# Performance work log

Hardware: AMD Instinct MI355X
Metric: run time of the kernel (lower is better)

Reference implementation:

```python
import jax, jax.numpy as jnp
import numpy as np

D_MODEL = 1024
N_HEADS = 16
HEAD_DIM = D_MODEL // N_HEADS


def setup_inputs() -> dict:
    key = jax.random.key(0)
    k1, k2, k3, k4, k5 = jax.random.split(key, 5)
    s = 1.0 / np.sqrt(D_MODEL)
    return {
        "x": jax.random.normal(k1, (2, 2048, D_MODEL), dtype=jnp.float32),
        "w_qkv": jax.random.normal(k2, (D_MODEL, 3 * D_MODEL), dtype=jnp.float32) * s,
        "b_qkv": jax.random.normal(k3, (3 * D_MODEL,), dtype=jnp.float32) * 0.02,
        "w_proj": jax.random.normal(k4, (D_MODEL, D_MODEL), dtype=jnp.float32) * s,
        "b_proj": jax.random.normal(k5, (D_MODEL,), dtype=jnp.float32) * 0.02,
    }


def reference(x, w_qkv, b_qkv, w_proj, b_proj):
    B, S, D = x.shape
    H, Hd = N_HEADS, HEAD_DIM
    qkv = x @ w_qkv + b_qkv                       # [B,S,3D]
    q, k, v = jnp.split(qkv, 3, axis=-1)
    # split heads -> [B,H,S,Hd]
    q = q.reshape(B, S, H, Hd).transpose(0, 2, 1, 3)
    k = k.reshape(B, S, H, Hd).transpose(0, 2, 1, 3)
    v = v.reshape(B, S, H, Hd).transpose(0, 2, 1, 3)
    scale = 1.0 / jnp.sqrt(jnp.asarray(Hd, dtype=x.dtype))
    scores = jnp.einsum("bhqd,bhkd->bhqk", q, k) * scale  # [B,H,S,S]
    causal = jnp.tril(jnp.ones((S, S), dtype=bool))
    scores = jnp.where(causal, scores, jnp.asarray(-jnp.inf, dtype=scores.dtype))
    attn = jax.nn.softmax(scores, axis=-1)
    out = jnp.einsum("bhqk,bhkd->bhqd", attn, v)  # [B,H,S,Hd]
    out = out.transpose(0, 2, 1, 3).reshape(B, S, D)
    return out @ w_proj + b_proj
```

## Files before the change

kernel.cpp:

```cpp
#include <hip/hip_runtime.h>


typedef float f32x4 __attribute__((ext_vector_type(4)));
typedef float f32x16 __attribute__((ext_vector_type(16)));
typedef short bf16x8 __attribute__((ext_vector_type(8)));

#if __has_builtin(__builtin_amdgcn_exp2f)
#define EXP2(x) __builtin_amdgcn_exp2f(x)
#else
#define EXP2(x) exp2f(x)
#endif

__device__ __forceinline__ unsigned short f2bf(float f) {
  union { float f; unsigned u; } v; v.f = f;
  unsigned u = v.u + 0x7fffu + ((v.u >> 16) & 1u);
  return (unsigned short)(u >> 16);
}

__device__ __forceinline__ void async_load16(const void* g, void* lds) {
  __builtin_amdgcn_global_load_lds(
      (const __attribute__((address_space(1))) void*)g,
      (__attribute__((address_space(3))) void*)lds, 16, 0, 0);
}

__global__ void f32_to_bf16_kernel(const float* __restrict__ in,
                                   unsigned short* __restrict__ out, int n) {
  int i = (blockIdx.x * 256 + threadIdx.x) * 4;
  if (i < n) {
    float4 f = *(const float4*)(in + i);
    ushort4 o;
    o.x = f2bf(f.x); o.y = f2bf(f.y); o.z = f2bf(f.z); o.w = f2bf(f.w);
    *(ushort4*)(out + i) = o;
  }
}

__global__ void transpose_f32_bf16_kernel(const float* __restrict__ in,
                                          unsigned short* __restrict__ out,
                                          int K, int N) {
  __shared__ float tile[32][33];
  int n0 = blockIdx.x * 32, k0 = blockIdx.y * 32;
  int tx = threadIdx.x, ty = threadIdx.y;
#pragma unroll
  for (int i = ty; i < 32; i += 8)
    tile[i][tx] = in[(size_t)(k0 + i) * N + (n0 + tx)];
  __syncthreads();
#pragma unroll
  for (int i = ty; i < 32; i += 8)
    out[(size_t)(n0 + i) * K + (k0 + tx)] = f2bf(tile[tx][i]);
}

template <int MI, int NI>
__device__ __forceinline__ void gemm_mainloop(
    const unsigned short* __restrict__ A,
    const unsigned short* __restrict__ BT,
    int K, int mBlk, int nBlk,
    unsigned short* As, unsigned short* Bs,
    f32x4 (&acc)[MI][NI], int lane, int wave)
{
  const int l16 = lane & 15, quad = lane >> 4;
  const int mW = (wave >> 1) * MI * 16;
  const int nW = (wave & 1) * NI * 16;
  constexpr int AROWS = 2 * MI * 16;
  constexpr int BROWS = 2 * NI * 16;
  constexpr int AINST = AROWS / 64;
  constexpr int BINST = BROWS / 64;
  const int rl = lane >> 2;
  const int cl = (lane & 3) * 8;

  for (int k0 = 0; k0 < K; k0 += 32) {
    __syncthreads();
#pragma unroll
    for (int t = 0; t < AINST; ++t) {
      const int rbase = wave * (AROWS / 4) + t * 16;
      async_load16(A + (size_t)(mBlk + rbase + rl) * K + k0 + cl, &As[rbase * 32]);
    }
#pragma unroll
    for (int t = 0; t < BINST; ++t) {
      const int rbase = wave * (BROWS / 4) + t * 16;
      async_load16(BT + (size_t)(nBlk + rbase + rl) * K + k0 + cl, &Bs[rbase * 32]);
    }
    __syncthreads();

    bf16x8 af[MI], bf[NI];
#pragma unroll
    for (int i = 0; i < MI; ++i)
      af[i] = *(const bf16x8*)&As[(mW + i * 16 + l16) * 32 + quad * 8];
#pragma unroll
    for (int j = 0; j < NI; ++j)
      bf[j] = *(const bf16x8*)&Bs[(nW + j * 16 + l16) * 32 + quad * 8];
#pragma unroll
    for (int i = 0; i < MI; ++i)
#pragma unroll
      for (int j = 0; j < NI; ++j)
        acc[i][j] = __builtin_amdgcn_mfma_f32_16x16x32_bf16(af[i], bf[j], acc[i][j], 0, 0, 0);
  }
}

__global__ __launch_bounds__(512, 2) void qkv_gemm_kernel(
    const unsigned short* __restrict__ A,
    const unsigned short* __restrict__ WT,
    const float* __restrict__ bias,
    unsigned short* __restrict__ QKV)
{
  __shared__ __align__(16) unsigned short Al[2][2][256][32];
  __shared__ __align__(16) unsigned short Bl[2][2][256][32];
  const int lane = threadIdx.x & 63;
  const int wave = threadIdx.x >> 6;
  const int l16 = lane & 15, quad = lane >> 4;
  const int wm = wave >> 2, wn = wave & 3;

  const int bid = blockIdx.x;
  const int xcd = bid & 7, rb = bid >> 3;
  const int bx = (xcd & 3) * 4 + (rb & 3);
  const int by = (xcd >> 2) * 6 + (rb >> 2);
  const int mBlk = bx * 256, nBlk = by * 256;

  const int srow = wave * 32 + (lane >> 2);
  const int scol = lane & 3;

  auto stage = [&](const unsigned short* __restrict__ G, int gRow0,
                   unsigned short (*L)[32], int kOff) {
#pragma unroll
    for (int i = 0; i < 2; ++i) {
      const int row = srow + i * 16;
      const int c = scol ^ ((row >> 1) & 3);
      async_load16(G + (size_t)(gRow0 + row) * 1024 + kOff + c * 8,
                   &L[wave * 32 + i * 16][0]);
    }
  };

  auto rdA = [&](int buf, int kh, int mi) -> bf16x8 {
    const int r = wm * 128 + mi * 16 + l16;
    return *(const bf16x8*)&Al[buf][kh][r][(quad ^ ((r >> 1) & 3)) * 8];
  };
  auto rdB = [&](int buf, int kh, int n) -> bf16x8 {
    const int r = wn * 64 + n * 16 + l16;
    return *(const bf16x8*)&Bl[buf][kh][r][(quad ^ ((r >> 1) & 3)) * 8];
  };

  f32x4 acc[8][4];
  const f32x4 z4 = {0.f, 0.f, 0.f, 0.f};
#pragma unroll
  for (int i = 0; i < 8; ++i)
#pragma unroll
    for (int j = 0; j < 4; ++j) acc[i][j] = z4;

  stage(A, mBlk, Al[0][0], 0);
  stage(WT, nBlk, Bl[0][0], 0);
  stage(A, mBlk, Al[0][1], 32);
  stage(WT, nBlk, Bl[0][1], 32);
  asm volatile("s_waitcnt vmcnt(4)\n\ts_barrier" ::: "memory");

  for (int t = 0; t < 16; ++t) {
    const int cur = t & 1, nxt = cur ^ 1;
    const int tn = (t + 1 < 16) ? t + 1 : 15;
    const int kO = tn * 64;
    bf16x8 bf[4], af[4];

    stage(A, mBlk, Al[nxt][0], kO);
#pragma unroll
    for (int n = 0; n < 4; ++n) bf[n] = rdB(cur, 0, n);
#pragma unroll
    for (int i = 0; i < 4; ++i) af[i] = rdA(cur, 0, i);
    asm volatile("s_barrier" ::: "memory");
    __builtin_amdgcn_s_setprio(1);
#pragma unroll
    for (int i = 0; i < 4; ++i)
#pragma unroll
      for (int n = 0; n < 4; ++n)
        acc[i][n] = __builtin_amdgcn_mfma_f32_16x16x32_bf16(af[i], bf[n], acc[i][n], 0, 0, 0);
    __builtin_amdgcn_s_setprio(0);
    asm volatile("s_barrier" ::: "memory");

    stage(WT, nBlk, Bl[nxt][0], kO);
#pragma unroll
    for (int i = 0; i < 4; ++i) af[i] = rdA(cur, 0, 4 + i);
    asm volatile("s_barrier" ::: "memory");
    __builtin_amdgcn_s_setprio(1);
#pragma unroll
    for (int i = 0; i < 4; ++i)
#pragma unroll
      for (int n = 0; n < 4; ++n)
        acc[4 + i][n] = __builtin_amdgcn_mfma_f32_16x16x32_bf16(af[i], bf[n], acc[4 + i][n], 0, 0, 0);
    __builtin_amdgcn_s_setprio(0);
    asm volatile("s_waitcnt vmcnt(4)\n\ts_barrier" ::: "memory");

    stage(A, mBlk, Al[nxt][1], kO + 32);
#pragma unroll
    for (int n = 0; n < 4; ++n) bf[n] = rdB(cur, 1, n);
#pragma unroll
    for (int i = 0; i < 4; ++i) af[i] = rdA(cur, 1, i);
    asm volatile("s_barrier" ::: "memory");
    __builtin_amdgcn_s_setprio(1);
#pragma unroll
    for (int i = 0; i < 4; ++i)
#pragma unroll
      for (int n = 0; n < 4; ++n)
        acc[i][n] = __builtin_amdgcn_mfma_f32_16x16x32_bf16(af[i], bf[n], acc[i][n], 0, 0, 0);
    __builtin_amdgcn_s_setprio(0);
    asm volatile("s_barrier" ::: "memory");

    stage(WT, nBlk, Bl[nxt][1], kO + 32);
#pragma unroll
    for (int i = 0; i < 4; ++i) af[i] = rdA(cur, 1, 4 + i);
    asm volatile("s_barrier" ::: "memory");
    __builtin_amdgcn_s_setprio(1);
#pragma unroll
    for (int i = 0; i < 4; ++i)
#pragma unroll
      for (int n = 0; n < 4; ++n)
        acc[4 + i][n] = __builtin_amdgcn_mfma_f32_16x16x32_bf16(af[i], bf[n], acc[4 + i][n], 0, 0, 0);
    __builtin_amdgcn_s_setprio(0);
    asm volatile("s_waitcnt vmcnt(4)\n\ts_barrier" ::: "memory");
  }
  asm volatile("s_waitcnt vmcnt(0)" ::: "memory");

  const int m0 = mBlk + wm * 128;
  const int n0 = nBlk + wn * 64;
  const int whichW = n0 >> 10;
  const int bb = m0 >> 11;
  const int sBase = (m0 & 2047);
  const size_t planeE = (size_t)2 * 16 * 2048 * 64;

  if (whichW == 2) {
    unsigned short* Vb = QKV + 2 * planeE;
#pragma unroll
    for (int j = 0; j < 4; ++j) {
      const int rem = (n0 & 1023) + j * 16 + l16;
      const int hh = rem >> 6, hd = rem & 63;
      const float bv = bias[n0 + j * 16 + l16];
      unsigned short* col = Vb + (((size_t)bb * 16 + hh) * 64 + hd) * 2048;
#pragma unroll
      for (int i = 0; i < 8; ++i) {
        unsigned short pk[4];
#pragma unroll
        for (int r = 0; r < 4; ++r) pk[r] = f2bf(acc[i][j][r] + bv);
        *(ushort4*)&col[sBase + i * 16 + quad * 4] = *(ushort4*)pk;
      }
    }
  } else {
    const float scale = (whichW == 0) ? 0.18033688011112042f : 1.0f;
#pragma unroll
    for (int j = 0; j < 4; ++j) {
      const int n = n0 + j * 16 + l16;
      const float bv = bias[n];
      const int rem = n & 1023;
      const int hh = rem >> 6, hd = rem & 63;
      unsigned short* pl = QKV + (size_t)whichW * planeE +
                           (((size_t)bb * 16 + hh) * 2048) * 64 + hd;
#pragma unroll
      for (int r = 0; r < 4; ++r) {
        const int s = sBase + (quad * 4 + r);
#pragma unroll
        for (int i = 0; i < 8; ++i)
          pl[(size_t)(s + i * 16) * 64] = f2bf((acc[i][j][r] + bv) * scale);
      }
    }
  }
}

__global__ __launch_bounds__(256, 2) void attn_kernel(
    const unsigned short* __restrict__ QKV,
    unsigned short* __restrict__ AO)
{
  __shared__ __align__(16) unsigned short Ks[3 * 64 * 64];
  __shared__ __align__(16) unsigned short Vs[3 * 64 * 64];
  const int lane = threadIdx.x & 63;
  const int wave = threadIdx.x >> 6;
  const int l31 = lane & 31;
  const int hi  = lane >> 5;

  const int lin  = blockIdx.x;
  const int xcd  = lin & 7;
  const int slot = lin >> 3;
  const int col  = xcd * 4 + (slot >> 4);
  const int b = col >> 4, h = col & 15;
  const int qg = (slot < 32) ? (slot & 15) : (15 - (slot & 15));
  const int qw = qg * 128 + wave * 32;

  const size_t planeE = (size_t)2 * 16 * 2048 * 64;
  const size_t bhS = ((size_t)b * 16 + h) * (size_t)(2048 * 64);
  const unsigned short* Q   = QKV + bhS;
  const unsigned short* Kg  = QKV + planeE + bhS;
  const unsigned short* VTg = QKV + 2 * planeE + bhS;

  bf16x8 qf_[4];
#pragma unroll
  for (int t = 0; t < 4; ++t)
    qf_[t] = *(const bf16x8*)(Q + (size_t)(qw + l31) * 64 + t * 16 + hi * 8);

  bf16x8 onesf;
#pragma unroll
  for (int i = 0; i < 8; ++i) onesf[i] = (short)0x3F80;

  f32x16 O[2], Osum;
#pragma unroll
  for (int r = 0; r < 16; ++r) { O[0][r] = 0.f; O[1][r] = 0.f; Osum[r] = 0.f; }

  const int tbase = (wave & 1) * 4;
  const bool doV = wave >= 2;

  auto stage = [&](int tileIdx, int bufIdx) {
    const int kt = tileIdx * 64;
    unsigned short* Kb = Ks + bufIdx * 4096;
    unsigned short* Vb = Vs + bufIdx * 4096;
#pragma unroll
    for (int i = 0; i < 4; ++i) {
      const int t = tbase + i;
      const int s = t * 64 + lane;
      const int row = s >> 3;
      const int c = (s & 7) ^ (row & 7);
      if (doV)
        async_load16(VTg + (size_t)row * 2048 + kt + c * 8, Vb + t * 512);
      else
        async_load16(Kg + (size_t)(kt + row) * 64 + c * 8, Kb + t * 512);
    }
  };

  const int nt = qg * 2 + 2;
  stage(0, 0);
  stage(1, 1);
  for (int ti = 0; ti < nt; ++ti) {
    asm volatile("s_waitcnt vmcnt(4)\n\ts_barrier" ::: "memory");
    const int tn = (ti + 2 < nt) ? ti + 2 : nt - 1;
    stage(tn, (ti + 2) % 3);
    const int kt = ti * 64;
    const unsigned short* Kb = Ks + (ti % 3) * 4096;
    const unsigned short* Vb = Vs + (ti % 3) * 4096;

    if (kt <= qw + 31) {
      const bool dmask = (kt + 63 > qw);
#pragma unroll
      for (int kg = 0; kg < 2; ++kg) {
        const int krow = kg * 32 + l31;
        const int ks7 = krow & 7;
        bf16x8 ka[4];
#pragma unroll
        for (int t = 0; t < 4; ++t)
          ka[t] = *(const bf16x8*)&Kb[(krow * 8 + ((t * 2 + hi) ^ ks7)) * 8];

        f32x16 sc;
#pragma unroll
        for (int r = 0; r < 16; ++r) sc[r] = 0.f;
        __builtin_amdgcn_s_setprio(1);
#pragma unroll
        for (int t = 0; t < 4; ++t)
          sc = __builtin_amdgcn_mfma_f32_32x32x16_bf16(ka[t], qf_[t], sc, 0, 0, 0);
        __builtin_amdgcn_s_setprio(0);

        float p[16];
#pragma unroll
        for (int r = 0; r < 16; ++r) {
          float v = sc[r];
          if (dmask) {
            const int key = kt + kg * 32 + (r & 3) + 8 * (r >> 2) + 4 * hi;
            if (key > qw + l31) v = -INFINITY;
          }
          p[r] = EXP2(v);
        }
        unsigned c8[8];
#pragma unroll
        for (int i = 0; i < 8; ++i)
          asm("v_cvt_pk_bf16_f32 %0, %1, %2"
              : "=v"(c8[i]) : "v"(p[2 * i]), "v"(p[2 * i + 1]));

#pragma unroll
        for (int half = 0; half < 2; ++half) {
          unsigned a0 = c8[4 * half + 0], a1 = c8[4 * half + 1];
          unsigned a2 = c8[4 * half + 2], a3 = c8[4 * half + 3];
          asm("v_permlane32_swap_b32 %0, %1" : "+v"(a0), "+v"(a2));
          asm("v_permlane32_swap_b32 %0, %1" : "+v"(a1), "+v"(a3));
          union { unsigned u[4]; bf16x8 v; } pa;
          pa.u[0] = a0; pa.u[1] = a1; pa.u[2] = a2; pa.u[3] = a3;
          const int kc = kg * 2 + half;

          __builtin_amdgcn_s_setprio(1);
          Osum = __builtin_amdgcn_mfma_f32_32x32x16_bf16(pa.v, onesf, Osum, 0, 0, 0);
#pragma unroll
          for (int g = 0; g < 2; ++g) {
            const int vrow = g * 32 + l31;
            bf16x8 vb = *(const bf16x8*)&Vb[(vrow * 8 + ((kc * 2 + hi) ^ (vrow & 7))) * 8];
            O[g] = __builtin_amdgcn_mfma_f32_32x32x16_bf16(pa.v, vb, O[g], 0, 0, 0);
          }
          __builtin_amdgcn_s_setprio(0);
        }
      }
    }
  }

  unsigned short* base = AO + ((size_t)b * 2048 + qw) * 1024 + h * 64 + l31;
#pragma unroll
  for (int r = 0; r < 16; ++r) {
    const float inv = 1.0f / Osum[r];
    const int row = (r & 3) + 8 * (r >> 2) + 4 * hi;
#pragma unroll
    for (int g = 0; g < 2; ++g)
      base[(size_t)row * 1024 + g * 32] = f2bf(O[g][r] * inv);
  }
}

__global__ __launch_bounds__(256) void proj_gemm_kernel(
    const unsigned short* __restrict__ A,
    const unsigned short* __restrict__ WT,
    const float* __restrict__ bias,
    float* __restrict__ out)
{
  __shared__ unsigned short As[64 * 32];
  __shared__ unsigned short Bs[128 * 32];
  const int lane = threadIdx.x & 63;
  const int wave = threadIdx.x >> 6;
  const int l16 = lane & 15, quad = lane >> 4;

  f32x4 acc[2][4];
  const f32x4 z4 = {0.f, 0.f, 0.f, 0.f};
#pragma unroll
  for (int i = 0; i < 2; ++i)
#pragma unroll
    for (int j = 0; j < 4; ++j) acc[i][j] = z4;

  gemm_mainloop<2, 4>(A, WT, 1024, blockIdx.x * 64, blockIdx.y * 128,
                      As, Bs, acc, lane, wave);

  const int m0 = blockIdx.x * 64 + (wave >> 1) * 32;
  const int n0 = blockIdx.y * 128 + (wave & 1) * 64;
#pragma unroll
  for (int i = 0; i < 2; ++i) {
#pragma unroll
    for (int j = 0; j < 4; ++j) {
      const int n = n0 + j * 16 + l16;
      const float bv = bias[n];
#pragma unroll
      for (int r = 0; r < 4; ++r) {
        const int m = m0 + i * 16 + quad * 4 + r;
        out[(size_t)m * 1024 + n] = acc[i][j][r] + bv;
      }
    }
  }
}

extern "C" void kernel_launch(void* const* d_in, const int* in_sizes, int n_in,
                              void* d_out, int out_size, void* d_ws, size_t ws_size,
                              hipStream_t stream) {
  const float* x      = (const float*)d_in[0];
  const float* w_qkv  = (const float*)d_in[1];
  const float* b_qkv  = (const float*)d_in[2];
  const float* w_proj = (const float*)d_in[3];
  const float* b_proj = (const float*)d_in[4];
  float* out = (float*)d_out;

  unsigned short* Xb  = (unsigned short*)d_ws;
  unsigned short* WTq = Xb + (size_t)4096 * 1024;
  unsigned short* WTp = WTq + (size_t)3072 * 1024;
  unsigned short* QKV = WTp + (size_t)1024 * 1024;
  unsigned short* AO  = QKV + (size_t)3 * 4096 * 1024;

  f32_to_bf16_kernel<<<4096, 256, 0, stream>>>(x, Xb, 4096 * 1024);
  transpose_f32_bf16_kernel<<<dim3(96, 32), dim3(32, 8), 0, stream>>>(w_qkv, WTq, 1024, 3072);
  transpose_f32_bf16_kernel<<<dim3(32, 32), dim3(32, 8), 0, stream>>>(w_proj, WTp, 1024, 1024);
  qkv_gemm_kernel<<<192, 512, 0, stream>>>(Xb, WTq, b_qkv, QKV);
  attn_kernel<<<512, 256, 0, stream>>>(QKV, AO);
  proj_gemm_kernel<<<dim3(64, 8), 256, 0, stream>>>(AO, WTp, b_proj, out);
}
```

Baseline: 203.3 us.

## Merge prep kernels into one launch and restructure QKV GEMM pipeline phases

Combines the x conversion and both weight-transpose kernels into a single prep kernel that picks its job from the block index, removing two launches and the gaps between them. In the QKV GEMM main loop, the four half-phases per K-step become two phases. Each phase issues both the A and B stage loads together, reads all eight A fragments, and runs 32 MFMAs with fewer barriers. The change raises register pressure (eight A fragments live at once) and alters the interleaving of global loads and compute, which may affect latency hiding.

```diff
diff --git a/kernel.cpp b/kernel.cpp
--- a/kernel.cpp
+++ b/kernel.cpp
@@ -23,30 +23,34 @@
       (__attribute__((address_space(3))) void*)lds, 16, 0, 0);
 }
 
-__global__ void f32_to_bf16_kernel(const float* __restrict__ in,
-                                   unsigned short* __restrict__ out, int n) {
-  int i = (blockIdx.x * 256 + threadIdx.x) * 4;
-  if (i < n) {
-    float4 f = *(const float4*)(in + i);
+__global__ __launch_bounds__(256) void prep_kernel(
+    const float* __restrict__ x, const float* __restrict__ w_qkv,
+    const float* __restrict__ w_proj, unsigned short* __restrict__ Xb,
+    unsigned short* __restrict__ WTq, unsigned short* __restrict__ WTp)
+{
+  const int bid = blockIdx.x;
+  const int tid = threadIdx.x;
+  if (bid < 4096) {
+    const int i = (bid * 256 + tid) * 4;
+    float4 f = *(const float4*)(x + i);
     ushort4 o;
     o.x = f2bf(f.x); o.y = f2bf(f.y); o.z = f2bf(f.z); o.w = f2bf(f.w);
-    *(ushort4*)(out + i) = o;
-  }
-}
-
-__global__ void transpose_f32_bf16_kernel(const float* __restrict__ in,
-                                          unsigned short* __restrict__ out,
-                                          int K, int N) {
-  __shared__ float tile[32][33];
-  int n0 = blockIdx.x * 32, k0 = blockIdx.y * 32;
-  int tx = threadIdx.x, ty = threadIdx.y;
-#pragma unroll
-  for (int i = ty; i < 32; i += 8)
-    tile[i][tx] = in[(size_t)(k0 + i) * N + (n0 + tx)];
-  __syncthreads();
-#pragma unroll
-  for (int i = ty; i < 32; i += 8)
-    out[(size_t)(n0 + i) * K + (k0 + tx)] = f2bf(tile[tx][i]);
+    *(ushort4*)(Xb + i) = o;
+  } else {
+    __shared__ float tile[32][33];
+    const float* in; unsigned short* out; int N, bx, by;
+    if (bid < 7168) { const int b2 = bid - 4096; in = w_qkv;  out = WTq; N = 3072; bx = b2 % 96; by = b2 / 96; }
+    else            { const int b3 = bid - 7168; in = w_proj; out = WTp; N = 1024; bx = b3 & 31; by = b3 >> 5; }
+    const int tx = tid & 31, ty = tid >> 5;
+    const int n0 = bx * 32, k0 = by * 32;
+#pragma unroll
+    for (int i = ty; i < 32; i += 8)
+      tile[i][tx] = in[(size_t)(k0 + i) * N + (n0 + tx)];
+    __syncthreads();
+#pragma unroll
+    for (int i = ty; i < 32; i += 8)
+      out[(size_t)(n0 + i) * 1024 + (k0 + tx)] = f2bf(tile[tx][i]);
+  }
 }
 
 template <int MI, int NI>
@@ -155,61 +159,35 @@
     const int cur = t & 1, nxt = cur ^ 1;
     const int tn = (t + 1 < 16) ? t + 1 : 15;
     const int kO = tn * 64;
-    bf16x8 bf[4], af[4];
+    bf16x8 bfr[4], afr[8];
 
     stage(A, mBlk, Al[nxt][0], kO);
-#pragma unroll
-    for (int n = 0; n < 4; ++n) bf[n] = rdB(cur, 0, n);
-#pragma unroll
-    for (int i = 0; i < 4; ++i) af[i] = rdA(cur, 0, i);
-    asm volatile("s_barrier" ::: "memory");
+    stage(WT, nBlk, Bl[nxt][0], kO);
+#pragma unroll
+    for (int n = 0; n < 4; ++n) bfr[n] = rdB(cur, 0, n);
+#pragma unroll
+    for (int i = 0; i < 8; ++i) afr[i] = rdA(cur, 0, i);
     __builtin_amdgcn_s_setprio(1);
 #pragma unroll
-    for (int i = 0; i < 4; ++i)
+    for (int i = 0; i < 8; ++i)
 #pragma unroll
       for (int n = 0; n < 4; ++n)
-        acc[i][n] = __builtin_amdgcn_mfma_f32_16x16x32_bf16(af[i], bf[n], acc[i][n], 0, 0, 0);
-    __builtin_amdgcn_s_setprio(0);
-    asm volatile("s_barrier" ::: "memory");
-
-    stage(WT, nBlk, Bl[nxt][0], kO);
-#pragma unroll
-    for (int i = 0; i < 4; ++i) af[i] = rdA(cur, 0, 4 + i);
-    asm volatile("s_barrier" ::: "memory");
-    __builtin_amdgcn_s_setprio(1);
-#pragma unroll
-    for (int i = 0; i < 4; ++i)
-#pragma unroll
-      for (int n = 0; n < 4; ++n)
-        acc[4 + i][n] = __builtin_amdgcn_mfma_f32_16x16x32_bf16(af[i], bf[n], acc[4 + i][n], 0, 0, 0);
+        acc[i][n] = __builtin_amdgcn_mfma_f32_16x16x32_bf16(afr[i], bfr[n], acc[i][n], 0, 0, 0);
     __builtin_amdgcn_s_setprio(0);
     asm volatile("s_waitcnt vmcnt(4)\n\ts_barrier" ::: "memory");
 
     stage(A, mBlk, Al[nxt][1], kO + 32);
-#pragma unroll
-    for (int n = 0; n < 4; ++n) bf[n] = rdB(cur, 1, n);
-#pragma unroll
-    for (int i = 0; i < 4; ++i) af[i] = rdA(cur, 1, i);
-    asm volatile("s_barrier" ::: "memory");
+    stage(WT, nBlk, Bl[nxt][1], kO + 32);
+#pragma unroll
+    for (int n = 0; n < 4; ++n) bfr[n] = rdB(cur, 1, n);
+#pragma unroll
+    for (int i = 0; i < 8; ++i) afr[i] = rdA(cur, 1, i);
     __builtin_amdgcn_s_setprio(1);
 #pragma unroll
-    for (int i = 0; i < 4; ++i)
+    for (int i = 0; i < 8; ++i)
 #pragma unroll
       for (int n = 0; n < 4; ++n)
-        acc[i][n] = __builtin_amdgcn_mfma_f32_16x16x32_bf16(af[i], bf[n], acc[i][n], 0, 0, 0);
-    __builtin_amdgcn_s_setprio(0);
-    asm volatile("s_barrier" ::: "memory");
-
-    stage(WT, nBlk, Bl[nxt][1], kO + 32);
-#pragma unroll
-    for (int i = 0; i < 4; ++i) af[i] = rdA(cur, 1, 4 + i);
-    asm volatile("s_barrier" ::: "memory");
-    __builtin_amdgcn_s_setprio(1);
-#pragma unroll
-    for (int i = 0; i < 4; ++i)
-#pragma unroll
-      for (int n = 0; n < 4; ++n)
-        acc[4 + i][n] = __builtin_amdgcn_mfma_f32_16x16x32_bf16(af[i], bf[n], acc[4 + i][n], 0, 0, 0);
+        acc[i][n] = __builtin_amdgcn_mfma_f32_16x16x32_bf16(afr[i], bfr[n], acc[i][n], 0, 0, 0);
     __builtin_amdgcn_s_setprio(0);
     asm volatile("s_waitcnt vmcnt(4)\n\ts_barrier" ::: "memory");
   }
@@ -454,9 +432,7 @@
   unsigned short* QKV = WTp + (size_t)1024 * 1024;
   unsigned short* AO  = QKV + (size_t)3 * 4096 * 1024;
 
-  f32_to_bf16_kernel<<<4096, 256, 0, stream>>>(x, Xb, 4096 * 1024);
-  transpose_f32_bf16_kernel<<<dim3(96, 32), dim3(32, 8), 0, stream>>>(w_qkv, WTq, 1024, 3072);
-  transpose_f32_bf16_kernel<<<dim3(32, 32), dim3(32, 8), 0, stream>>>(w_proj, WTp, 1024, 1024);
+  prep_kernel<<<8192, 256, 0, stream>>>(x, w_qkv, w_proj, Xb, WTq, WTp);
   qkv_gemm_kernel<<<192, 512, 0, stream>>>(Xb, WTq, b_qkv, QKV);
   attn_kernel<<<512, 256, 0, stream>>>(QKV, AO);
   proj_gemm_kernel<<<dim3(64, 8), 256, 0, stream>>>(AO, WTp, b_proj, out);
```

Result: faster. 195.8 us (-3.7%).
